# Kernel optimization log

Hardware: AMD Instinct MI355X
Metric: run time of the kernel (lower is better)

The kernel has to match this reference:

```python
import jax, jax.numpy as jnp
import numpy as np

B, T, S, A, U = 128, 512, 64, 8, 512  # batch, episode len, state dim, n_actions, n_units


def setup_inputs() -> dict:
    key = jax.random.key(0)
    ks = jax.random.split(key, 10)
    IN = S + A
    return {
        "states": jax.random.normal(ks[0], (B, T + 1, S), jnp.float32),
        "actions": jax.random.randint(ks[1], (B, T), 0, A),
        # cell-input gate: feedforward weights only, init N(0, 0.1)
        "W_ci": jax.random.normal(ks[2], (IN, U), jnp.float32) * 0.1,
        "b_ci": jax.random.normal(ks[3], (U,), jnp.float32),
        # input gate: recurrent weights only, init N(0, 0.1); bias mean -3
        "W_ig": jax.random.normal(ks[4], (U, U), jnp.float32) * 0.1,
        "b_ig": jax.random.normal(ks[5], (U,), jnp.float32) - 3.0,
        # output gate: feedforward weights only, init N(0, 0.1)
        "W_og": jax.random.normal(ks[6], (IN, U), jnp.float32) * 0.1,
        "b_og": jax.random.normal(ks[7], (U,), jnp.float32),
        # output head Linear(n_units, 1)
        "W_lin": jax.random.normal(ks[8], (U, 1), jnp.float32) * (1.0 / np.sqrt(U)),
        "b_lin": jnp.zeros((1,), jnp.float32),
    }


def reference(states, actions, W_ci, b_ci, W_ig, b_ig, W_og, b_og, W_lin, b_lin):
    Bv, T1, _ = states.shape
    # one-hot actions [B,T,A], pad one zero timestep -> [B,T+1,A]
    acts = jax.nn.one_hot(actions, A, dtype=states.dtype)
    acts = jnp.concatenate([acts, jnp.zeros((Bv, 1, A), states.dtype)], axis=1)
    x = jnp.concatenate([states, acts], axis=2)  # [B, T+1, S+A]

    # feedforward-only gates computed for all timesteps at once
    ci = jnp.tanh(jnp.einsum('bti,iu->btu', x, W_ci) + b_ci)          # cell input
    og = jax.nn.sigmoid(jnp.einsum('bti,iu->btu', x, W_og) + b_og)   # output gate

    def step(carry, inputs):
        c, h = carry
        ci_t, og_t = inputs
        ig = jax.nn.sigmoid(h @ W_ig + b_ig)  # recurrent-only input gate
        c = c + ci_t * ig                     # no forget gate: fg == 1
        h = c * og_t                          # a_out = identity
        return (c, h), h

    zeros = jnp.zeros((Bv, U), states.dtype)
    _, h_seq = jax.lax.scan(step, (zeros, zeros),
                            (jnp.swapaxes(ci, 0, 1), jnp.swapaxes(og, 0, 1)))
    h = jnp.swapaxes(h_seq, 0, 1)  # [B, T+1, U]
    return h @ W_lin + b_lin       # [B, T+1, 1]
```

## Files before the change

### kernel.cpp

```cpp
#include <hip/hip_runtime.h>
#include <cstdint>

#define NBATCH 128
#define NT 512
#define NT1 513
#define NS 64
#define NU 512
#define NBW 16
#define KF_SHORTS 16384
#define KF_V8 (KF_SHORTS / 8)
#define PACK_SHORTS (16 * KF_SHORTS)
#define CIOG_BYTES ((size_t)NT1 * NBATCH * NU * 4)
#define KF_ST 12
#define KF_LD 4
#define DYN_LDS (KF_LD * KF_SHORTS * 2)

typedef __attribute__((ext_vector_type(8))) short short8_t;
typedef __attribute__((ext_vector_type(4))) float f32x4;

__device__ __forceinline__ float sigf(float z) {
    return 1.0f / (1.0f + __expf(-z));
}
__device__ __forceinline__ float tanh_fast(float z) {
    return 2.0f / (1.0f + __expf(-2.0f * z)) - 1.0f;
}
__device__ __forceinline__ uint32_t bf16_top(float f) {
    uint32_t u = __float_as_uint(f);
    u += 0x7FFFu + ((u >> 16) & 1u);
    return u & 0xFFFF0000u;
}
__device__ __forceinline__ float f_from_lo(uint32_t p) { return __uint_as_float(p << 16); }
__device__ __forceinline__ float f_from_hi(uint32_t p) { return __uint_as_float(p & 0xFFFF0000u); }

__global__ __launch_bounds__(512) void pack_kernel(
    const float* __restrict__ W_ig, short* __restrict__ pack)
{
    const int g = blockIdx.x * 512 + threadIdx.x;
    const int lane = g & 63;
    const int nf = (g >> 6) & 3;
    const int wv = (g >> 8) & 7;
    const int kf = g >> 11;
    const int r16 = lane & 15, kg = lane >> 4;
    const int u = wv * 64 + nf * 16 + r16;
    const int kb = kf * 32 + kg * 8;
    short8_t w;
    #pragma unroll
    for (int j = 0; j < 8; ++j) {
        w[j] = (short)(bf16_top(W_ig[(size_t)(kb + j) * NU + u]) >> 16);
    }
    *(short8_t*)(pack + (size_t)g * 8) = w;
}

__global__ __launch_bounds__(512) void ff_kernel(
    const float* __restrict__ states, const int* __restrict__ actions,
    const float* __restrict__ W_ci, const float* __restrict__ b_ci,
    const float* __restrict__ W_og, const float* __restrict__ b_og,
    uint32_t* __restrict__ ciog)
{
    __shared__ __align__(16) float sh_s[32][64];
    __shared__ int sh_a[32];
    const int tid = threadIdx.x;
    const int b = blockIdx.x / 17;
    const int t0 = (blockIdx.x % 17) * 32;
    const int tcnt = (t0 + 32 <= NT1) ? 32 : (NT1 - t0);

    const float* sp = states + ((size_t)b * NT1 + t0) * NS;
    for (int j = tid; j < tcnt * 16; j += 512) {
        const float4 v = *(const float4*)(sp + j * 4);
        *(float4*)&sh_s[j >> 4][(j & 15) * 4] = v;
    }
    for (int tt = tid; tt < tcnt; tt += 512) {
        const int t = t0 + tt;
        sh_a[tt] = (t < NT) ? actions[b * NT + t] : -1;
    }
    __syncthreads();

    const int u = tid;
    float accc[32], acco[32];
    const float bc = b_ci[u], bo = b_og[u];
    #pragma unroll
    for (int tt = 0; tt < 32; ++tt) { accc[tt] = bc; acco[tt] = bo; }

    for (int i = 0; i < NS; ++i) {
        const float wc = W_ci[(size_t)i * NU + u];
        const float wo = W_og[(size_t)i * NU + u];
        #pragma unroll
        for (int tt = 0; tt < 32; ++tt) {
            const float s = sh_s[tt][i];
            accc[tt] = fmaf(s, wc, accc[tt]);
            acco[tt] = fmaf(s, wo, acco[tt]);
        }
    }
    #pragma unroll
    for (int tt = 0; tt < 32; ++tt) {
        if (tt < tcnt) {
            float zc = accc[tt], zo = acco[tt];
            const int a = sh_a[tt];
            if (a >= 0) {
                zc += W_ci[(size_t)(NS + a) * NU + u];
                zo += W_og[(size_t)(NS + a) * NU + u];
            }
            const float ci = tanh_fast(zc);
            const float og = sigf(zo);
            ciog[((size_t)(t0 + tt) * NBATCH + b) * NU + u] = bf16_top(og) | (bf16_top(ci) >> 16);
        }
    }
}

__global__ __launch_bounds__(512) void rec_stream4(
    const short* __restrict__ pack,
    const float* __restrict__ b_ig, const float* __restrict__ W_lin,
    const float* __restrict__ b_lin,
    const uint32_t* __restrict__ ciog,
    float* __restrict__ out)
{
    extern __shared__ __align__(16) char dynsm[];
    __shared__ __align__(16) short hsh[NBW * NU];
    __shared__ float ysum[2][8][NBW];

    const int tid  = threadIdx.x;
    const int lane = tid & 63;
    const int wv   = tid >> 6;
    const int n0   = wv << 6;
    const int r16  = lane & 15;
    const int kg   = lane >> 4;
    const int b0   = blockIdx.x * NBW;

    const short8_t* pr = (const short8_t*)pack;
    #define PIDX(KF_, NF_) (((((KF_) * 8) + wv) * 4 + (NF_)) * 64 + lane)
    #define LD4(S_, KF_) { (S_)[0] = pr[PIDX(KF_, 0)]; (S_)[1] = pr[PIDX(KF_, 1)]; \
                           (S_)[2] = pr[PIDX(KF_, 2)]; (S_)[3] = pr[PIDX(KF_, 3)]; }

    short8_t* dl = (short8_t*)dynsm;
    {
        const short8_t* pl = pr + KF_ST * KF_V8;
        #pragma unroll
        for (int i = 0; i < 16; ++i) dl[i * 512 + tid] = pl[i * 512 + tid];
    }

    float big[4], wl[4];
    #pragma unroll
    for (int nf = 0; nf < 4; ++nf) {
        big[nf] = b_ig[n0 + nf * 16 + r16];
        wl[nf]  = W_lin[n0 + nf * 16 + r16];
    }
    const float blin = b_lin[0];

    for (int i = tid; i < NBW * NU; i += 512) hsh[i] = 0;

    float cst[4][4] = {{0.f,0.f,0.f,0.f},{0.f,0.f,0.f,0.f},
                       {0.f,0.f,0.f,0.f},{0.f,0.f,0.f,0.f}};

    const int amask = (r16 & 7) << 4;
    const char* hb = (const char*)hsh;
    char* hw = (char*)hsh;

    short8_t S0[4], S1[4];
    LD4(S0, 0) LD4(S1, 1)

    __syncthreads();

    for (int t = 0; t < NT1; ++t) {
        if (t > 0 && wv == 0 && lane < NBW) {
            float y = blin;
            #pragma unroll
            for (int w8 = 0; w8 < 8; ++w8) y += ysum[(t - 1) & 1][w8][lane];
            out[(size_t)(b0 + lane) * NT1 + (t - 1)] = y;
        }

        f32x4 acc[4];
        #pragma unroll
        for (int nf = 0; nf < 4; ++nf) { acc[nf][0]=0.f; acc[nf][1]=0.f; acc[nf][2]=0.f; acc[nf][3]=0.f; }

        #define AFRAG(KF) (*(const short8_t*)(hb + r16 * 1024 + ((((KF) * 64) + kg * 16) ^ amask)))
        #define MF4(KF, W) { const short8_t a_ = AFRAG(KF); \
            acc[0] = __builtin_amdgcn_mfma_f32_16x16x32_bf16(a_, (W)[0], acc[0], 0, 0, 0); \
            acc[1] = __builtin_amdgcn_mfma_f32_16x16x32_bf16(a_, (W)[1], acc[1], 0, 0, 0); \
            acc[2] = __builtin_amdgcn_mfma_f32_16x16x32_bf16(a_, (W)[2], acc[2], 0, 0, 0); \
            acc[3] = __builtin_amdgcn_mfma_f32_16x16x32_bf16(a_, (W)[3], acc[3], 0, 0, 0); }

        MF4(0,  S0)  LD4(S0, 2)
        MF4(1,  S1)  LD4(S1, 3)
        MF4(2,  S0)  LD4(S0, 4)
        MF4(3,  S1)  LD4(S1, 5)
        MF4(4,  S0)  LD4(S0, 6)
        MF4(5,  S1)  LD4(S1, 7)
        MF4(6,  S0)  LD4(S0, 8)
        MF4(7,  S1)  LD4(S1, 9)
        MF4(8,  S0)  LD4(S0, 10)
        MF4(9,  S1)  LD4(S1, 11)
        MF4(10, S0)  LD4(S0, 0)
        MF4(11, S1)  LD4(S1, 1)

        #pragma unroll
        for (int kf = 0; kf < KF_LD; ++kf) {
            short8_t wt[4];
            #pragma unroll
            for (int nf = 0; nf < 4; ++nf)
                wt[nf] = dl[((kf * 8 + wv) * 4 + nf) * 64 + lane];
            MF4(KF_ST + kf, wt)
        }
        #undef MF4
        #undef AFRAG

        __syncthreads();

        uint32_t pk[4][4];
        {
            const uint32_t* cg = ciog + (size_t)t * (NBATCH * NU);
            #pragma unroll
            for (int nf = 0; nf < 4; ++nf) {
                #pragma unroll
                for (int j = 0; j < 4; ++j)
                    pk[nf][j] = cg[(size_t)(b0 + kg * 4 + j) * NU + n0 + nf * 16 + r16];
            }
        }

        float yp[4] = {0.f, 0.f, 0.f, 0.f};
        #pragma unroll
        for (int nf = 0; nf < 4; ++nf) {
            const int u2 = (n0 + nf * 16 + r16) * 2;
            #pragma unroll
            for (int j = 0; j < 4; ++j) {
                const int b = kg * 4 + j;
                const float z   = acc[nf][j] + big[nf];
                const float igv = sigf(z);
                const uint32_t p = pk[nf][j];
                cst[nf][j] = fmaf(f_from_lo(p), igv, cst[nf][j]);
                const float hv = cst[nf][j] * f_from_hi(p);
                yp[j] = fmaf(hv, wl[nf], yp[j]);
                const int wb = b * 1024 + (u2 ^ ((b & 7) << 4));
                *(short*)(hw + wb) = (short)(bf16_top(hv) >> 16);
            }
        }

        #pragma unroll
        for (int m = 1; m <= 8; m <<= 1) {
            yp[0] += __shfl_xor(yp[0], m);
            yp[1] += __shfl_xor(yp[1], m);
            yp[2] += __shfl_xor(yp[2], m);
            yp[3] += __shfl_xor(yp[3], m);
        }
        if (r16 == 0) {
            #pragma unroll
            for (int j = 0; j < 4; ++j) ysum[t & 1][wv][kg * 4 + j] = yp[j];
        }

        __syncthreads();
    }

    if (wv == 0 && lane < NBW) {
        float y = blin;
        #pragma unroll
        for (int w8 = 0; w8 < 8; ++w8) y += ysum[0][w8][lane];
        out[(size_t)(b0 + lane) * NT1 + NT] = y;
    }
    #undef LD4
    #undef PIDX
}

__device__ __forceinline__ void fma4(float4& acc, const float4 w, const float s) {
    acc.x = fmaf(w.x, s, acc.x);
    acc.y = fmaf(w.y, s, acc.y);
    acc.z = fmaf(w.z, s, acc.z);
    acc.w = fmaf(w.w, s, acc.w);
}

__global__ __launch_bounds__(512) void rec_fallback(
    const float* __restrict__ states, const int* __restrict__ actions,
    const float* __restrict__ W_ci, const float* __restrict__ b_ci,
    const float* __restrict__ W_ig, const float* __restrict__ b_ig,
    const float* __restrict__ W_og, const float* __restrict__ b_og,
    const float* __restrict__ W_lin, const float* __restrict__ b_lin,
    float* __restrict__ out)
{
    __shared__ __align__(16) float h_lds[2][NU];
    __shared__ __align__(16) float part[4][2][NU];
    __shared__ float ysum[8][2];
    __shared__ float x_lds[2][NS];
    __shared__ int a_lds[2];

    const int tid = threadIdx.x;
    const int b0 = blockIdx.x * 2;
    const int uq = tid & 127;
    const int kq = tid >> 7;
    const int k0 = kq << 7;

    h_lds[0][tid] = 0.0f;
    h_lds[1][tid] = 0.0f;
    float c0 = 0.0f, c1 = 0.0f;
    const float wlin = W_lin[tid];
    const float big_ = b_ig[tid];
    const float blin = b_lin[0];
    const float bc = b_ci[tid], bo = b_og[tid];
    __syncthreads();

    for (int t = 0; t < NT1; ++t) {
        if (tid < 128) {
            const int bb = tid >> 6, i = tid & 63;
            x_lds[bb][i] = states[((size_t)(b0 + bb) * NT1 + t) * NS + i];
        } else if (tid < 130) {
            const int bb = tid - 128;
            a_lds[bb] = (t < NT) ? actions[(b0 + bb) * NT + t] : -1;
        }

        float4 a0 = make_float4(0.f, 0.f, 0.f, 0.f);
        float4 a1 = make_float4(0.f, 0.f, 0.f, 0.f);
        for (int kk = 0; kk < 128; kk += 4) {
            const int k = k0 + kk;
            const float4 h0v = *(const float4*)&h_lds[0][k];
            const float4 h1v = *(const float4*)&h_lds[1][k];
            const float* wr = W_ig + (size_t)k * NU + (uq << 2);
            const float4 w0 = *(const float4*)(wr);
            const float4 w1 = *(const float4*)(wr + NU);
            const float4 w2 = *(const float4*)(wr + 2 * NU);
            const float4 w3 = *(const float4*)(wr + 3 * NU);
            fma4(a0, w0, h0v.x); fma4(a1, w0, h1v.x);
            fma4(a0, w1, h0v.y); fma4(a1, w1, h1v.y);
            fma4(a0, w2, h0v.z); fma4(a1, w2, h1v.z);
            fma4(a0, w3, h0v.w); fma4(a1, w3, h1v.w);
        }
        *(float4*)&part[kq][0][uq << 2] = a0;
        *(float4*)&part[kq][1][uq << 2] = a1;
        __syncthreads();

        float z0 = big_, z1 = big_;
        #pragma unroll
        for (int q = 0; q < 4; ++q) { z0 += part[q][0][tid]; z1 += part[q][1][tid]; }

        float zc0 = bc, zo0 = bo, zc1 = bc, zo1 = bo;
        for (int i = 0; i < NS; ++i) {
            const float wc = W_ci[(size_t)i * NU + tid];
            const float wo = W_og[(size_t)i * NU + tid];
            const float s0v = x_lds[0][i];
            const float s1v = x_lds[1][i];
            zc0 = fmaf(s0v, wc, zc0); zo0 = fmaf(s0v, wo, zo0);
            zc1 = fmaf(s1v, wc, zc1); zo1 = fmaf(s1v, wo, zo1);
        }
        const int a0i = a_lds[0], a1i = a_lds[1];
        if (a0i >= 0) { zc0 += W_ci[(size_t)(NS + a0i) * NU + tid]; zo0 += W_og[(size_t)(NS + a0i) * NU + tid]; }
        if (a1i >= 0) { zc1 += W_ci[(size_t)(NS + a1i) * NU + tid]; zo1 += W_og[(size_t)(NS + a1i) * NU + tid]; }
        const float ci0 = tanh_fast(zc0), og0 = sigf(zo0);
        const float ci1 = tanh_fast(zc1), og1 = sigf(zo1);

        const float ig0 = sigf(z0), ig1 = sigf(z1);
        c0 = fmaf(ci0, ig0, c0);
        c1 = fmaf(ci1, ig1, c1);
        const float h0 = c0 * og0, h1 = c1 * og1;
        h_lds[0][tid] = h0;
        h_lds[1][tid] = h1;

        float y0 = h0 * wlin, y1 = h1 * wlin;
        #pragma unroll
        for (int off = 32; off > 0; off >>= 1) {
            y0 += __shfl_xor(y0, off);
            y1 += __shfl_xor(y1, off);
        }
        if ((tid & 63) == 0) { ysum[tid >> 6][0] = y0; ysum[tid >> 6][1] = y1; }
        __syncthreads();

        if (tid < 2) {
            float y = blin;
            #pragma unroll
            for (int w = 0; w < 8; ++w) y += ysum[w][tid];
            out[(size_t)(b0 + tid) * NT1 + t] = y;
        }
    }
}

extern "C" void kernel_launch(void* const* d_in, const int* in_sizes, int n_in,
                              void* d_out, int out_size, void* d_ws, size_t ws_size,
                              hipStream_t stream) {
    const float* states = (const float*)d_in[0];
    const int*   actions= (const int*)d_in[1];
    const float* W_ci = (const float*)d_in[2];
    const float* b_ci = (const float*)d_in[3];
    const float* W_ig = (const float*)d_in[4];
    const float* b_ig = (const float*)d_in[5];
    const float* W_og = (const float*)d_in[6];
    const float* b_og = (const float*)d_in[7];
    const float* W_lin= (const float*)d_in[8];
    const float* b_lin= (const float*)d_in[9];
    float* out = (float*)d_out;

    const size_t need = CIOG_BYTES + (size_t)PACK_SHORTS * 2;
    if (ws_size >= need) {
        uint32_t* ciog = (uint32_t*)d_ws;
        short* pack = (short*)((char*)d_ws + CIOG_BYTES);

        (void)hipFuncSetAttribute((const void*)rec_stream4,
                                  hipFuncAttributeMaxDynamicSharedMemorySize, DYN_LDS);

        pack_kernel<<<dim3(64), dim3(512), 0, stream>>>(W_ig, pack);
        ff_kernel<<<dim3(NBATCH * 17), dim3(512), 0, stream>>>(
            states, actions, W_ci, b_ci, W_og, b_og, ciog);
        rec_stream4<<<dim3(NBATCH / NBW), dim3(512), DYN_LDS, stream>>>(
            pack, b_ig, W_lin, b_lin, ciog, out);
    } else {
        rec_fallback<<<dim3(NBATCH / 2), dim3(512), 0, stream>>>(
            states, actions, W_ci, b_ci, W_ig, b_ig, W_og, b_og, W_lin, b_lin, out);
    }
}
```

Measured before the change: 3.527 ms.

## Widen recurrent kernel to 16 waves and prefetch gate inputs mid-matmul

The recurrent kernel now runs 1024 threads (16 waves), each owning 32 output units instead of 64. The packed weight layout is regenerated to match, with two N-fragments per wave instead of four. Each wave issues half as many MFMAs per step, shortening the serial per-timestep critical path. The per-step ci/og global loads are moved between the MFMA groups to hide their latency, at the cost of more waves in barriers and a 16-way ysum reduction.

```diff
diff --git a/kernel.cpp b/kernel.cpp
--- a/kernel.cpp
+++ b/kernel.cpp
@@ -37,11 +37,11 @@
 {
     const int g = blockIdx.x * 512 + threadIdx.x;
     const int lane = g & 63;
-    const int nf = (g >> 6) & 3;
-    const int wv = (g >> 8) & 7;
+    const int nf = (g >> 6) & 1;
+    const int wv = (g >> 7) & 15;
     const int kf = g >> 11;
     const int r16 = lane & 15, kg = lane >> 4;
-    const int u = wv * 64 + nf * 16 + r16;
+    const int u = wv * 32 + nf * 16 + r16;
     const int kb = kf * 32 + kg * 8;
     short8_t w;
     #pragma unroll
@@ -107,7 +107,7 @@
     }
 }
 
-__global__ __launch_bounds__(512) void rec_stream4(
+__global__ __launch_bounds__(1024) void rec_wide(
     const short* __restrict__ pack,
     const float* __restrict__ b_ig, const float* __restrict__ W_lin,
     const float* __restrict__ b_lin,
@@ -116,47 +116,45 @@
 {
     extern __shared__ __align__(16) char dynsm[];
     __shared__ __align__(16) short hsh[NBW * NU];
-    __shared__ float ysum[2][8][NBW];
+    __shared__ float ysum[2][16][NBW];
 
     const int tid  = threadIdx.x;
     const int lane = tid & 63;
     const int wv   = tid >> 6;
-    const int n0   = wv << 6;
+    const int n0   = wv << 5;
     const int r16  = lane & 15;
     const int kg   = lane >> 4;
     const int b0   = blockIdx.x * NBW;
 
     const short8_t* pr = (const short8_t*)pack;
-    #define PIDX(KF_, NF_) (((((KF_) * 8) + wv) * 4 + (NF_)) * 64 + lane)
-    #define LD4(S_, KF_) { (S_)[0] = pr[PIDX(KF_, 0)]; (S_)[1] = pr[PIDX(KF_, 1)]; \
-                           (S_)[2] = pr[PIDX(KF_, 2)]; (S_)[3] = pr[PIDX(KF_, 3)]; }
+    #define PIDX(KF_, NF_) (((((KF_) * 16) + wv) * 2 + (NF_)) * 64 + lane)
+    #define LD2(S_, KF_) { (S_)[0] = pr[PIDX(KF_, 0)]; (S_)[1] = pr[PIDX(KF_, 1)]; }
 
     short8_t* dl = (short8_t*)dynsm;
     {
         const short8_t* pl = pr + KF_ST * KF_V8;
         #pragma unroll
-        for (int i = 0; i < 16; ++i) dl[i * 512 + tid] = pl[i * 512 + tid];
-    }
-
-    float big[4], wl[4];
+        for (int i = 0; i < 8; ++i) dl[i * 1024 + tid] = pl[i * 1024 + tid];
+    }
+
+    float big[2], wl[2];
     #pragma unroll
-    for (int nf = 0; nf < 4; ++nf) {
+    for (int nf = 0; nf < 2; ++nf) {
         big[nf] = b_ig[n0 + nf * 16 + r16];
         wl[nf]  = W_lin[n0 + nf * 16 + r16];
     }
     const float blin = b_lin[0];
 
-    for (int i = tid; i < NBW * NU; i += 512) hsh[i] = 0;
-
-    float cst[4][4] = {{0.f,0.f,0.f,0.f},{0.f,0.f,0.f,0.f},
-                       {0.f,0.f,0.f,0.f},{0.f,0.f,0.f,0.f}};
+    for (int i = tid; i < NBW * NU; i += 1024) hsh[i] = 0;
+
+    float cst[2][4] = {{0.f,0.f,0.f,0.f},{0.f,0.f,0.f,0.f}};
 
     const int amask = (r16 & 7) << 4;
     const char* hb = (const char*)hsh;
     char* hw = (char*)hsh;
 
-    short8_t S0[4], S1[4];
-    LD4(S0, 0) LD4(S1, 1)
+    short8_t S0[2], S1[2];
+    LD2(S0, 0) LD2(S1, 1)
 
     __syncthreads();
 
@@ -164,61 +162,60 @@
         if (t > 0 && wv == 0 && lane < NBW) {
             float y = blin;
             #pragma unroll
-            for (int w8 = 0; w8 < 8; ++w8) y += ysum[(t - 1) & 1][w8][lane];
+            for (int w16 = 0; w16 < 16; ++w16) y += ysum[(t - 1) & 1][w16][lane];
             out[(size_t)(b0 + lane) * NT1 + (t - 1)] = y;
         }
 
-        f32x4 acc[4];
-        #pragma unroll
-        for (int nf = 0; nf < 4; ++nf) { acc[nf][0]=0.f; acc[nf][1]=0.f; acc[nf][2]=0.f; acc[nf][3]=0.f; }
+        f32x4 acc[2];
+        #pragma unroll
+        for (int nf = 0; nf < 2; ++nf) { acc[nf][0]=0.f; acc[nf][1]=0.f; acc[nf][2]=0.f; acc[nf][3]=0.f; }
 
         #define AFRAG(KF) (*(const short8_t*)(hb + r16 * 1024 + ((((KF) * 64) + kg * 16) ^ amask)))
-        #define MF4(KF, W) { const short8_t a_ = AFRAG(KF); \
+        #define MF2(KF, W) { const short8_t a_ = AFRAG(KF); \
             acc[0] = __builtin_amdgcn_mfma_f32_16x16x32_bf16(a_, (W)[0], acc[0], 0, 0, 0); \
-            acc[1] = __builtin_amdgcn_mfma_f32_16x16x32_bf16(a_, (W)[1], acc[1], 0, 0, 0); \
-            acc[2] = __builtin_amdgcn_mfma_f32_16x16x32_bf16(a_, (W)[2], acc[2], 0, 0, 0); \
-            acc[3] = __builtin_amdgcn_mfma_f32_16x16x32_bf16(a_, (W)[3], acc[3], 0, 0, 0); }
-
-        MF4(0,  S0)  LD4(S0, 2)
-        MF4(1,  S1)  LD4(S1, 3)
-        MF4(2,  S0)  LD4(S0, 4)
-        MF4(3,  S1)  LD4(S1, 5)
-        MF4(4,  S0)  LD4(S0, 6)
-        MF4(5,  S1)  LD4(S1, 7)
-        MF4(6,  S0)  LD4(S0, 8)
-        MF4(7,  S1)  LD4(S1, 9)
-        MF4(8,  S0)  LD4(S0, 10)
-        MF4(9,  S1)  LD4(S1, 11)
-        MF4(10, S0)  LD4(S0, 0)
-        MF4(11, S1)  LD4(S1, 1)
-
-        #pragma unroll
-        for (int kf = 0; kf < KF_LD; ++kf) {
-            short8_t wt[4];
-            #pragma unroll
-            for (int nf = 0; nf < 4; ++nf)
-                wt[nf] = dl[((kf * 8 + wv) * 4 + nf) * 64 + lane];
-            MF4(KF_ST + kf, wt)
-        }
-        #undef MF4
-        #undef AFRAG
-
-        __syncthreads();
-
-        uint32_t pk[4][4];
+            acc[1] = __builtin_amdgcn_mfma_f32_16x16x32_bf16(a_, (W)[1], acc[1], 0, 0, 0); }
+
+        MF2(0,  S0)  LD2(S0, 2)
+        MF2(1,  S1)  LD2(S1, 3)
+        MF2(2,  S0)  LD2(S0, 4)
+        MF2(3,  S1)  LD2(S1, 5)
+        MF2(4,  S0)  LD2(S0, 6)
+        MF2(5,  S1)  LD2(S1, 7)
+        MF2(6,  S0)  LD2(S0, 8)
+        MF2(7,  S1)  LD2(S1, 9)
+
+        uint32_t pk[2][4];
         {
             const uint32_t* cg = ciog + (size_t)t * (NBATCH * NU);
             #pragma unroll
-            for (int nf = 0; nf < 4; ++nf) {
+            for (int nf = 0; nf < 2; ++nf) {
                 #pragma unroll
                 for (int j = 0; j < 4; ++j)
                     pk[nf][j] = cg[(size_t)(b0 + kg * 4 + j) * NU + n0 + nf * 16 + r16];
             }
         }
 
+        MF2(8,  S0)  LD2(S0, 10)
+        MF2(9,  S1)  LD2(S1, 11)
+        MF2(10, S0)  LD2(S0, 0)
+        MF2(11, S1)  LD2(S1, 1)
+
+        #pragma unroll
+        for (int kf = 0; kf < KF_LD; ++kf) {
+            short8_t wt[2];
+            #pragma unroll
+            for (int nf = 0; nf < 2; ++nf)
+                wt[nf] = dl[((kf * 16 + wv) * 2 + nf) * 64 + lane];
+            MF2(KF_ST + kf, wt)
+        }
+        #undef MF2
+        #undef AFRAG
+
+        __syncthreads();
+
         float yp[4] = {0.f, 0.f, 0.f, 0.f};
         #pragma unroll
-        for (int nf = 0; nf < 4; ++nf) {
+        for (int nf = 0; nf < 2; ++nf) {
             const int u2 = (n0 + nf * 16 + r16) * 2;
             #pragma unroll
             for (int j = 0; j < 4; ++j) {
@@ -252,10 +249,10 @@
     if (wv == 0 && lane < NBW) {
         float y = blin;
         #pragma unroll
-        for (int w8 = 0; w8 < 8; ++w8) y += ysum[0][w8][lane];
+        for (int w16 = 0; w16 < 16; ++w16) y += ysum[0][w16][lane];
         out[(size_t)(b0 + lane) * NT1 + NT] = y;
     }
-    #undef LD4
+    #undef LD2
     #undef PIDX
 }
 
@@ -388,13 +385,13 @@
         uint32_t* ciog = (uint32_t*)d_ws;
         short* pack = (short*)((char*)d_ws + CIOG_BYTES);
 
-        (void)hipFuncSetAttribute((const void*)rec_stream4,
+        (void)hipFuncSetAttribute((const void*)rec_wide,
                                   hipFuncAttributeMaxDynamicSharedMemorySize, DYN_LDS);
 
         pack_kernel<<<dim3(64), dim3(512), 0, stream>>>(W_ig, pack);
         ff_kernel<<<dim3(NBATCH * 17), dim3(512), 0, stream>>>(
             states, actions, W_ci, b_ci, W_og, b_og, ciog);
-        rec_stream4<<<dim3(NBATCH / NBW), dim3(512), DYN_LDS, stream>>>(
+        rec_wide<<<dim3(NBATCH / NBW), dim3(1024), DYN_LDS, stream>>>(
             pack, b_ig, W_lin, b_lin, ciog, out);
     } else {
         rec_fallback<<<dim3(NBATCH / 2), dim3(512), 0, stream>>>(
```

Result: slower. 3.763 ms (+6.7%).
